# Performance work log

Measured on AMD Instinct MI355X. Metric: run time of the kernel, lower is better.

Reference implementation:

```python
import jax, jax.numpy as jnp
import numpy as np

TEMPERATURE = 0.07
EPS = 1e-12  # F.normalize clamp


def _project(x, We, be, W1, b1, W2, b2):
    # encoder Linear then projection head Linear->ReLU->Linear
    h = x @ We + be                      # [B, 512]
    h = jax.nn.relu(h @ W1 + b1)         # [B, 256]
    return h @ W2 + b2                   # [B, 128]


def _ntxent(z1, z2, t):
    B = z1.shape[0]
    z1 = z1 / jnp.maximum(jnp.linalg.norm(z1, axis=1, keepdims=True), EPS)
    z2 = z2 / jnp.maximum(jnp.linalg.norm(z2, axis=1, keepdims=True), EPS)
    reps = jnp.concatenate([z1, z2], axis=0)          # [2B, 128]
    sim = reps @ reps.T                               # [2B, 2B]
    N = 2 * B
    idx = jnp.arange(N)
    # positives: eye rolled by B along columns -> column (i+B) mod N
    pos = sim[idx, (idx + B) % N][:, None]            # [N, 1]
    # negatives: all off-diagonal entries per row, in column order
    cols = jnp.arange(N - 1)[None, :]                 # [1, N-1]
    neg_idx = cols + (cols >= idx[:, None])           # skip the diagonal
    neg = jnp.take_along_axis(sim, neg_idx, axis=1)   # [N, N-1]
    logits = jnp.concatenate([pos, neg], axis=1) / t  # [N, N]
    # cross-entropy with label 0
    return jnp.mean(jax.nn.logsumexp(logits, axis=1) - logits[:, 0])


def setup_inputs() -> dict:
    key = jax.random.key(0)
    ks = jax.random.split(key, 10)
    B, Din, Denc, Dh, Dp = 4096, 1024, 512, 256, 128
    s = lambda fan_in: 1.0 / np.sqrt(fan_in)
    return {
        "x_image": jax.random.normal(ks[0], (B, Din), jnp.float32),
        "x_text": jax.random.normal(ks[1], (B, Din), jnp.float32),
        "We_img": jax.random.normal(ks[2], (Din, Denc), jnp.float32) * s(Din),
        "be_img": jnp.zeros((Denc,), jnp.float32),
        "We_txt": jax.random.normal(ks[3], (Din, Denc), jnp.float32) * s(Din),
        "be_txt": jnp.zeros((Denc,), jnp.float32),
        "Wp1_img": jax.random.normal(ks[4], (Denc, Dh), jnp.float32) * s(Denc),
        "bp1_img": jnp.zeros((Dh,), jnp.float32),
        "Wp2_img": jax.random.normal(ks[5], (Dh, Dp), jnp.float32) * s(Dh),
        "bp2_img": jnp.zeros((Dp,), jnp.float32),
        "Wp1_txt": jax.random.normal(ks[6], (Denc, Dh), jnp.float32) * s(Denc),
        "bp1_txt": jnp.zeros((Dh,), jnp.float32),
        "Wp2_txt": jax.random.normal(ks[7], (Dh, Dp), jnp.float32) * s(Dh),
        "bp2_txt": jnp.zeros((Dp,), jnp.float32),
    }


def reference(x_image, x_text, We_img, be_img, We_txt, be_txt,
              Wp1_img, bp1_img, Wp2_img, bp2_img,
              Wp1_txt, bp1_txt, Wp2_txt, bp2_txt):
    z1 = _project(x_image, We_img, be_img, Wp1_img, bp1_img, Wp2_img, bp2_img)
    z2 = _project(x_text, We_txt, be_txt, Wp1_txt, bp1_txt, Wp2_txt, bp2_txt)
    # single modality pair ('image','text') -> one NT-Xent loss
    return _ntxent(z1, z2, TEMPERATURE)
```

## Files before the change

kernel.cpp:

```cpp
#include <hip/hip_runtime.h>
#include <hip/hip_bf16.h>
#include <math.h>

typedef __bf16 bf16_t;
typedef __bf16 bf8 __attribute__((ext_vector_type(8)));
typedef __bf16 bf4 __attribute__((ext_vector_type(4)));
typedef float f32x4 __attribute__((ext_vector_type(4)));
typedef int i32x8 __attribute__((ext_vector_type(8)));
typedef unsigned char u8;

#define AS1 __attribute__((address_space(1)))
#define AS3 __attribute__((address_space(3)))

#define B_ROWS 4096
#define NTOT   8192
#define DIN    1024
#define DENC   512
#define DH     256
#define DP     128
#define NSLICE 64
#define INV_T        14.285714285714286f
#define SCALE_LOG2   20.609929155556620f

__device__ __forceinline__ f32x4 mfma_16x16x32(bf8 a, bf8 b, f32x4 c) {
  return __builtin_amdgcn_mfma_f32_16x16x32_bf16(a, b, c, 0, 0, 0);
}

__global__ __launch_bounds__(256) void prep_kernel(
    const float* __restrict__ x_i, const float* __restrict__ x_t,
    const float* __restrict__ We_i, const float* __restrict__ We_t,
    const float* __restrict__ W1_i, const float* __restrict__ W1_t,
    const float* __restrict__ W2_i, const float* __restrict__ W2_t,
    bf16_t* __restrict__ xb_i, bf16_t* __restrict__ xb_t,
    bf16_t* __restrict__ Wet_i, bf16_t* __restrict__ Wet_t,
    bf16_t* __restrict__ W1t_i, bf16_t* __restrict__ W1t_t,
    bf16_t* __restrict__ W2t_i, bf16_t* __restrict__ W2t_t) {
  const int b = blockIdx.x;
  const int tid = threadIdx.x;
  if (b >= 336) {
    int idx = (b - 336) * 256 + tid;
    const int HALF = (B_ROWS * DIN) / 4;
    const float* s; bf16_t* d; int off;
    if (idx < HALF) { s = x_i; d = xb_i; off = idx; }
    else            { s = x_t; d = xb_t; off = idx - HALF; }
    float4 v = ((const float4*)s)[off];
    bf4 w = { (bf16_t)v.x, (bf16_t)v.y, (bf16_t)v.z, (bf16_t)v.w };
    ((bf4*)d)[off] = w;
    return;
  }
  const float* src; bf16_t* dst; int K, N, tile;
  if (b < 128)      { src = We_i; dst = Wet_i; K = 1024; N = 512; tile = b; }
  else if (b < 256) { src = We_t; dst = Wet_t; K = 1024; N = 512; tile = b - 128; }
  else if (b < 288) { src = W1_i; dst = W1t_i; K = 512;  N = 256; tile = b - 256; }
  else if (b < 320) { src = W1_t; dst = W1t_t; K = 512;  N = 256; tile = b - 288; }
  else if (b < 328) { src = W2_i; dst = W2t_i; K = 256;  N = 128; tile = b - 320; }
  else              { src = W2_t; dst = W2t_t; K = 256;  N = 128; tile = b - 328; }
  const int tilesN = N >> 6;
  const int k0 = (tile / tilesN) * 64;
  const int n0 = (tile % tilesN) * 64;

  __shared__ float ld[64][65];
  #pragma unroll
  for (int i = 0; i < 4; ++i) {
    int cid = tid + i * 256;
    int r = cid >> 4;
    int c = (cid & 15) * 4;
    float4 v = *(const float4*)(src + (size_t)(k0 + r) * N + n0 + c);
    ld[r][c + 0] = v.x; ld[r][c + 1] = v.y; ld[r][c + 2] = v.z; ld[r][c + 3] = v.w;
  }
  __syncthreads();
  #pragma unroll
  for (int i = 0; i < 2; ++i) {
    int cid = tid + i * 256;
    int rn = cid >> 3;
    int c8 = (cid & 7) * 8;
    bf8 w;
    #pragma unroll
    for (int j = 0; j < 8; ++j) w[j] = (bf16_t)ld[c8 + j][rn];
    *(bf8*)(dst + (size_t)(n0 + rn) * K + k0 + c8) = w;
  }
}

template<int MT, bool RELU>
__global__ __launch_bounds__(256) void gemm_glds(
    const bf16_t* __restrict__ A0, const bf16_t* __restrict__ A1,
    const bf16_t* __restrict__ B0, const bf16_t* __restrict__ B1,
    const float* __restrict__ bias0, const float* __restrict__ bias1,
    bf16_t* __restrict__ out0, bf16_t* __restrict__ out1,
    int N, int K) {
  const bf16_t* A   = blockIdx.z ? A1 : A0;
  const bf16_t* Bt  = blockIdx.z ? B1 : B0;
  const float* bias = blockIdx.z ? bias1 : bias0;
  bf16_t* outp      = blockIdx.z ? out1 : out0;

  const int nb   = blockIdx.x * 64;
  const int mb   = blockIdx.y * MT;
  const int tid  = threadIdx.x;
  const int wave = tid >> 6;
  const int lane = tid & 63;
  const int l15  = lane & 15;
  const int quad = lane >> 4;
  constexpr int CH = MT / 64;

  __shared__ __align__(16) bf16_t As[3][MT * 32];
  __shared__ __align__(16) bf16_t Bs[3][64 * 32];

  f32x4 acc[CH][4];
  #pragma unroll
  for (int i = 0; i < CH; ++i)
    #pragma unroll
    for (int j = 0; j < 4; ++j) acc[i][j] = (f32x4){0.f, 0.f, 0.f, 0.f};

  auto stage = [&](int k0, int pb) {
    #pragma unroll
    for (int i = 0; i < CH; ++i) {
      const int s = tid + i * 256;
      const bf16_t* ga = A + (size_t)(mb + (s >> 2)) * K + k0 + (s & 3) * 8;
      __builtin_amdgcn_global_load_lds(
          (const AS1 void*)ga,
          (AS3 void*)(As[pb] + (size_t)(wave * 64 + i * 256) * 8), 16, 0, 0);
    }
    const bf16_t* gb = Bt + (size_t)(nb + (tid >> 2)) * K + k0 + (tid & 3) * 8;
    __builtin_amdgcn_global_load_lds(
        (const AS1 void*)gb,
        (AS3 void*)(Bs[pb] + (size_t)(wave * 64) * 8), 16, 0, 0);
  };

  const int T = K >> 5;
  stage(0, 0);
  stage(32, 1);
  for (int t = 0; t < T; ++t) {
    if (t == T - 1) {
      asm volatile("s_waitcnt vmcnt(0)" ::: "memory");
    } else if constexpr (CH == 2) {
      asm volatile("s_waitcnt vmcnt(3)" ::: "memory");
    } else {
      asm volatile("s_waitcnt vmcnt(2)" ::: "memory");
    }
    __builtin_amdgcn_s_barrier();
    if (t + 2 < T) stage((t + 2) << 5, (t + 2) % 3);
    const bf16_t* as = As[t % 3];
    const bf16_t* bs = Bs[t % 3];
    bf8 a[CH];
    #pragma unroll
    for (int i = 0; i < CH; ++i)
      a[i] = *(const bf8*)(as + (size_t)(wave * (16 * CH) + i * 16 + l15) * 32 + quad * 8);
    #pragma unroll
    for (int nt = 0; nt < 4; ++nt) {
      bf8 bb = *(const bf8*)(bs + (size_t)(nt * 16 + l15) * 32 + quad * 8);
      #pragma unroll
      for (int i = 0; i < CH; ++i)
        acc[i][nt] = mfma_16x16x32(a[i], bb, acc[i][nt]);
    }
  }

  #pragma unroll
  for (int i = 0; i < CH; ++i) {
    const int orow = mb + wave * (16 * CH) + i * 16 + quad * 4;
    #pragma unroll
    for (int nt = 0; nt < 4; ++nt) {
      const int ocol = nb + nt * 16 + l15;
      const float bval = bias[ocol];
      #pragma unroll
      for (int r = 0; r < 4; ++r) {
        float v = acc[i][nt][r] + bval;
        if (RELU) v = fmaxf(v, 0.f);
        outp[(size_t)(orow + r) * N + ocol] = (bf16_t)v;
      }
    }
  }
}

__global__ __launch_bounds__(256) void head2_norm(
    const bf16_t* __restrict__ A0, const bf16_t* __restrict__ A1,
    const bf16_t* __restrict__ B0, const bf16_t* __restrict__ B1,
    const float* __restrict__ bias0, const float* __restrict__ bias1,
    u8* __restrict__ reps8) {
  const bf16_t* A   = blockIdx.z ? A1 : A0;
  const bf16_t* Bt  = blockIdx.z ? B1 : B0;
  const float* bias = blockIdx.z ? bias1 : bias0;

  const int mb   = blockIdx.x * 16;
  const int tid  = threadIdx.x;
  const int wave = tid >> 6;
  const int lane = tid & 63;
  const int l15  = lane & 15;
  const int quad = lane >> 4;
  const int wc0  = wave * 32;

  __shared__ __align__(16) bf16_t Asb[8 * 16 * 32];
  __shared__ __align__(16) bf16_t Bsb[8 * 128 * 32];
  __shared__ float ssL[64];

  #pragma unroll
  for (int i = 0; i < 2; ++i) {
    const int s = i * 256 + tid;
    const int kt = s >> 6, slot = s & 63;
    const int row = slot >> 2, j = slot & 3, cf = j ^ (row & 3);
    const bf16_t* ga = A + (size_t)(mb + row) * DH + kt * 32 + cf * 8;
    __builtin_amdgcn_global_load_lds(
        (const AS1 void*)ga,
        (AS3 void*)(Asb + (size_t)(i * 256 + wave * 64) * 8), 16, 0, 0);
  }
  #pragma unroll
  for (int i = 0; i < 16; ++i) {
    const int s2 = i * 256 + tid;
    const int kt = s2 >> 9, slot = s2 & 511;
    const int col = slot >> 2, j = slot & 3, cf = j ^ (col & 3);
    const bf16_t* gb = Bt + (size_t)col * DH + kt * 32 + cf * 8;
    __builtin_amdgcn_global_load_lds(
        (const AS1 void*)gb,
        (AS3 void*)(Bsb + (size_t)(i * 256 + wave * 64) * 8), 16, 0, 0);
  }
  __syncthreads();

  f32x4 acc[2];
  acc[0] = (f32x4){0.f, 0.f, 0.f, 0.f};
  acc[1] = (f32x4){0.f, 0.f, 0.f, 0.f};
  #pragma unroll
  for (int kt = 0; kt < 8; ++kt) {
    bf8 a = *(const bf8*)(Asb + (size_t)kt * 512 +
                          (size_t)(l15 * 4 + (quad ^ (l15 & 3))) * 8);
    #pragma unroll
    for (int nt = 0; nt < 2; ++nt) {
      const int col = wc0 + nt * 16 + l15;
      bf8 bb = *(const bf8*)(Bsb + (size_t)kt * 4096 +
                             (size_t)(col * 4 + (quad ^ (col & 3))) * 8);
      acc[nt] = mfma_16x16x32(a, bb, acc[nt]);
    }
  }

  float ssp[4];
  #pragma unroll
  for (int r = 0; r < 4; ++r) {
    #pragma unroll
    for (int nt = 0; nt < 2; ++nt) acc[nt][r] += bias[wc0 + nt * 16 + l15];
    float s = acc[0][r] * acc[0][r] + acc[1][r] * acc[1][r];
    s += __shfl_xor(s, 1); s += __shfl_xor(s, 2);
    s += __shfl_xor(s, 4); s += __shfl_xor(s, 8);
    ssp[r] = s;
  }
  if (l15 == 0) {
    #pragma unroll
    for (int r = 0; r < 4; ++r) ssL[wave * 16 + quad * 4 + r] = ssp[r];
  }
  __syncthreads();
  const size_t gr0 = (size_t)(blockIdx.z ? B_ROWS : 0) + mb + quad * 4;
  #pragma unroll
  for (int r = 0; r < 4; ++r) {
    const int row = quad * 4 + r;
    float tot = ssL[row] + ssL[16 + row] + ssL[32 + row] + ssL[48 + row];
    const float inv = 1.0f / fmaxf(sqrtf(tot), 1e-12f);
    int pk = __builtin_amdgcn_cvt_pk_fp8_f32(acc[0][r] * inv, acc[1][r] * inv, 0, 0);
    reps8[(gr0 + r) * DP + wc0 + l15]      = (u8)(pk & 0xff);
    reps8[(gr0 + r) * DP + wc0 + 16 + l15] = (u8)((pk >> 8) & 0xff);
  }
}

__global__ __launch_bounds__(256, 4) void sim_fp8_kernel(
    const u8* __restrict__ reps8, float* __restrict__ Spart) {
  const int l = blockIdx.x;
  int by = (int)((65.0f - sqrtf(4225.0f - 4.0f * (float)l)) * 0.5f);
  while ((by + 1) * (65 - (by + 1)) <= l) ++by;
  while (by * (65 - by) > l) --by;
  const int bxh = 2 * by + (l - by * (65 - by));
  const bool diag = (bxh - 2 * by) < 2;
  const int rowbase = by * 256;
  const int col0    = bxh * 128;
  const int tid  = threadIdx.x;
  const int wave = tid >> 6;
  const int lane = tid & 63;
  const int l15  = lane & 15;
  const int quad = lane >> 4;

  __shared__ __align__(16) u8 Bs[2][64 * DP];
  __shared__ float csw[4][128];

  const int r0 = rowbase + wave * 64;
  i32x8 af[4];
  #pragma unroll
  for (int c = 0; c < 4; ++c) {
    const uint4* ap = (const uint4*)(reps8 + (size_t)(r0 + c * 16 + l15) * DP + quad * 32);
    uint4 x0 = ap[0], x1 = ap[1];
    af[c] = (i32x8){(int)x0.x, (int)x0.y, (int)x0.z, (int)x0.w,
                    (int)x1.x, (int)x1.y, (int)x1.z, (int)x1.w};
  }

  float rs[4][4];
  #pragma unroll
  for (int c = 0; c < 4; ++c)
    #pragma unroll
    for (int r = 0; r < 4; ++r) rs[c][r] = 0.f;

  auto stage = [&](int t, int pb) {
    const int jt0 = col0 + t * 64;
    #pragma unroll
    for (int i = 0; i < 2; ++i) {
      const int s   = i * 256 + tid;
      const int col = s >> 3;
      const int cf  = (s & 7) ^ (col & 7);
      const u8* g = reps8 + (size_t)(jt0 + col) * DP + cf * 16;
      __builtin_amdgcn_global_load_lds(
          (const AS1 void*)g,
          (AS3 void*)(Bs[pb] + (size_t)(i * 256 + wave * 64) * 16), 16, 0, 0);
    }
  };

  stage(0, 0);
  for (int t = 0; t < 2; ++t) {
    __syncthreads();
    if (t == 0) stage(1, 1);
    const u8* buf = Bs[t & 1];

    #pragma unroll
    for (int g = 0; g < 2; ++g) {
      f32x4 pacc[2][4];
      __builtin_amdgcn_s_setprio(1);
      #pragma unroll
      for (int h = 0; h < 2; ++h) {
        const int st = g * 2 + h;
        const int coln = st * 16 + l15;
        const u8* cbase = buf + (size_t)coln * DP;
        const int c0 = ((2 * quad)     ^ (coln & 7)) * 16;
        const int c1 = ((2 * quad + 1) ^ (coln & 7)) * 16;
        uint4 b0 = *(const uint4*)(cbase + c0);
        uint4 b1 = *(const uint4*)(cbase + c1);
        i32x8 bf = (i32x8){(int)b0.x, (int)b0.y, (int)b0.z, (int)b0.w,
                           (int)b1.x, (int)b1.y, (int)b1.z, (int)b1.w};
        #pragma unroll
        for (int c = 0; c < 4; ++c) {
          pacc[h][c] = __builtin_amdgcn_mfma_scale_f32_16x16x128_f8f6f4(
              af[c], bf, (f32x4){0.f, 0.f, 0.f, 0.f}, 0, 0, 0,
              0x7F7F7F7F, 0, 0x7F7F7F7F);
        }
      }
      __builtin_amdgcn_s_setprio(0);

      #pragma unroll
      for (int h = 0; h < 2; ++h) {
        float csp[4] = {0.f, 0.f, 0.f, 0.f};
        #pragma unroll
        for (int c = 0; c < 4; ++c) {
          #pragma unroll
          for (int r = 0; r < 4; ++r) {
            float ev = __builtin_amdgcn_exp2f(pacc[h][c][r] * SCALE_LOG2);
            rs[c][r] += ev;
            csp[r] += ev;
          }
        }
        if (!diag) {
          float cs = (csp[0] + csp[1]) + (csp[2] + csp[3]);
          cs += __shfl_xor(cs, 16);
          cs += __shfl_xor(cs, 32);
          if (quad == 0) csw[wave][t * 64 + (g * 2 + h) * 16 + l15] = cs;
        }
      }
    }
  }

  #pragma unroll
  for (int c = 0; c < 4; ++c) {
    const int i0 = r0 + c * 16 + quad * 4;
    #pragma unroll
    for (int r = 0; r < 4; ++r) {
      float v = rs[c][r];
      v += __shfl_xor(v, 1); v += __shfl_xor(v, 2);
      v += __shfl_xor(v, 4); v += __shfl_xor(v, 8);
      if (l15 == 0) Spart[(size_t)bxh * NTOT + i0 + r] = v;
    }
  }

  if (!diag) {
    __syncthreads();
    if (tid < 128) {
      Spart[(size_t)(2 * by) * NTOT + col0 + tid] = csw[0][tid] + csw[1][tid];
    } else {
      const int j = tid - 128;
      Spart[(size_t)(2 * by + 1) * NTOT + col0 + j] = csw[2][j] + csw[3][j];
    }
  }
}

__global__ __launch_bounds__(256) void rowfinal_kernel(
    const u8* __restrict__ reps8, const float* __restrict__ Spart,
    float* __restrict__ L) {
  const int tid  = threadIdx.x;
  const int wave = tid >> 6;
  const int lane = tid & 63;
  const int row  = blockIdx.x * 4 + wave;
  const int ua = *(const unsigned short*)(reps8 + (size_t)row * DP + lane * 2);
  const int ub = *(const unsigned short*)(reps8 + (size_t)(row ^ B_ROWS) * DP + lane * 2);
  float a0 = __builtin_amdgcn_cvt_f32_fp8(ua, 0);
  float a1 = __builtin_amdgcn_cvt_f32_fp8(ua, 1);
  float b0 = __builtin_amdgcn_cvt_f32_fp8(ub, 0);
  float b1 = __builtin_amdgcn_cvt_f32_fp8(ub, 1);
  float dii = a0 * a0 + a1 * a1;
  float pos = a0 * b0 + a1 * b1;
  float ps  = Spart[(size_t)lane * NTOT + row];
  #pragma unroll
  for (int m = 1; m < 64; m <<= 1) {
    dii += __shfl_xor(dii, m);
    pos += __shfl_xor(pos, m);
    ps  += __shfl_xor(ps, m);
  }
  if (lane == 0) {
    float Si = ps - __builtin_amdgcn_exp2f(dii * SCALE_LOG2)
                  + __builtin_amdgcn_exp2f(pos * SCALE_LOG2);
    L[row] = logf(Si) - pos * INV_T;
  }
}

__global__ __launch_bounds__(1024) void reduce_kernel(
    const float* __restrict__ L, float* __restrict__ out) {
  const int tid = threadIdx.x;
  float acc = 0.f;
  for (int i = tid; i < NTOT; i += 1024) acc += L[i];
  #pragma unroll
  for (int m = 1; m < 64; m <<= 1) acc += __shfl_xor(acc, m);
  __shared__ float wsum[16];
  if ((tid & 63) == 0) wsum[tid >> 6] = acc;
  __syncthreads();
  if (tid < 16) {
    float v = wsum[tid];
    #pragma unroll
    for (int m = 1; m < 16; m <<= 1) v += __shfl_xor(v, m);
    if (tid == 0) out[0] = v * (1.0f / NTOT);
  }
}

extern "C" void kernel_launch(void* const* d_in, const int* in_sizes, int n_in,
                              void* d_out, int out_size, void* d_ws, size_t ws_size,
                              hipStream_t stream) {
  const float* x_img  = (const float*)d_in[0];
  const float* x_txt  = (const float*)d_in[1];
  const float* We_img = (const float*)d_in[2];
  const float* be_img = (const float*)d_in[3];
  const float* We_txt = (const float*)d_in[4];
  const float* be_txt = (const float*)d_in[5];
  const float* W1_img = (const float*)d_in[6];
  const float* b1_img = (const float*)d_in[7];
  const float* W2_img = (const float*)d_in[8];
  const float* b2_img = (const float*)d_in[9];
  const float* W1_txt = (const float*)d_in[10];
  const float* b1_txt = (const float*)d_in[11];
  const float* W2_txt = (const float*)d_in[12];
  const float* b2_txt = (const float*)d_in[13];

  char* p = (char*)d_ws;
  bf16_t* xbf_img = (bf16_t*)p; p += (size_t)B_ROWS * DIN * 2;
  bf16_t* xbf_txt = (bf16_t*)p; p += (size_t)B_ROWS * DIN * 2;
  bf16_t* Wet_img = (bf16_t*)p; p += (size_t)DENC * DIN * 2;
  bf16_t* Wet_txt = (bf16_t*)p; p += (size_t)DENC * DIN * 2;
  bf16_t* W1t_img = (bf16_t*)p; p += (size_t)DH * DENC * 2;
  bf16_t* W1t_txt = (bf16_t*)p; p += (size_t)DH * DENC * 2;
  bf16_t* W2t_img = (bf16_t*)p; p += (size_t)DP * DH * 2;
  bf16_t* W2t_txt = (bf16_t*)p; p += (size_t)DP * DH * 2;
  bf16_t* h_img   = (bf16_t*)p; p += (size_t)B_ROWS * DENC * 2;
  bf16_t* h_txt   = (bf16_t*)p; p += (size_t)B_ROWS * DENC * 2;
  bf16_t* g_img   = (bf16_t*)p; p += (size_t)B_ROWS * DH * 2;
  bf16_t* g_txt   = (bf16_t*)p; p += (size_t)B_ROWS * DH * 2;
  u8*     reps8   = (u8*)    p; p += (size_t)NTOT * DP;
  float*  Spart   = (float*) p; p += (size_t)NSLICE * NTOT * 4;
  float*  L       = (float*) p; p += (size_t)NTOT * 4;

  prep_kernel<<<336 + 8192, 256, 0, stream>>>(
      x_img, x_txt, We_img, We_txt, W1_img, W1_txt, W2_img, W2_txt,
      xbf_img, xbf_txt, Wet_img, Wet_txt, W1t_img, W1t_txt, W2t_img, W2t_txt);

  gemm_glds<128, false><<<dim3(DENC / 64, B_ROWS / 128, 2), 256, 0, stream>>>(
      xbf_img, xbf_txt, Wet_img, Wet_txt, be_img, be_txt, h_img, h_txt,
      DENC, DIN);
  gemm_glds<64, true><<<dim3(DH / 64, B_ROWS / 64, 2), 256, 0, stream>>>(
      h_img, h_txt, W1t_img, W1t_txt, b1_img, b1_txt, g_img, g_txt,
      DH, DENC);
  head2_norm<<<dim3(B_ROWS / 16, 1, 2), 256, 0, stream>>>(
      g_img, g_txt, W2t_img, W2t_txt, b2_img, b2_txt, reps8);

  sim_fp8_kernel<<<dim3(1056), 256, 0, stream>>>(reps8, Spart);
  rowfinal_kernel<<<NTOT / 4, 256, 0, stream>>>(reps8, Spart, L);
  reduce_kernel<<<1, 1024, 0, stream>>>(L, (float*)d_out);
}
```

Measured before the change: 182.2 us.

## Fuse projection head layers, fold final reduction into rowfinal, coarsen cast blocks

Merges the W1 GEMM+ReLU and the W2 GEMM+normalize into one per-16-row kernel that keeps the hidden activation in LDS, so the intermediate g tensor is never written to or read from global memory. The final mean reduction moves into the rowfinal kernel through a last-block atomic counter, which removes a launch but adds a memset. The input cast now processes four float4 elements per thread with a quarter of the blocks. The fused head kernel uses small 16-row tiles and reloads the full W1 for every block, and it synchronizes on each k-step, which may leave the MFMA units underused.

```diff
diff --git a/kernel.cpp b/kernel.cpp
--- a/kernel.cpp
+++ b/kernel.cpp
@@ -25,6 +25,7 @@
 __device__ __forceinline__ f32x4 mfma_16x16x32(bf8 a, bf8 b, f32x4 c) {
   return __builtin_amdgcn_mfma_f32_16x16x32_bf16(a, b, c, 0, 0, 0);
 }
+
 
 __global__ __launch_bounds__(256) void prep_kernel(
     const float* __restrict__ x_i, const float* __restrict__ x_t,
@@ -38,14 +39,18 @@
   const int b = blockIdx.x;
   const int tid = threadIdx.x;
   if (b >= 336) {
-    int idx = (b - 336) * 256 + tid;
+    const int base = (b - 336) * 256 + tid;
     const int HALF = (B_ROWS * DIN) / 4;
-    const float* s; bf16_t* d; int off;
-    if (idx < HALF) { s = x_i; d = xb_i; off = idx; }
-    else            { s = x_t; d = xb_t; off = idx - HALF; }
-    float4 v = ((const float4*)s)[off];
-    bf4 w = { (bf16_t)v.x, (bf16_t)v.y, (bf16_t)v.z, (bf16_t)v.w };
-    ((bf4*)d)[off] = w;
+    #pragma unroll
+    for (int it = 0; it < 4; ++it) {
+      int idx = base + it * (2048 * 256);
+      const float* s; bf16_t* d; int off;
+      if (idx < HALF) { s = x_i; d = xb_i; off = idx; }
+      else            { s = x_t; d = xb_t; off = idx - HALF; }
+      float4 v = ((const float4*)s)[off];
+      bf4 w = { (bf16_t)v.x, (bf16_t)v.y, (bf16_t)v.z, (bf16_t)v.w };
+      ((bf4*)d)[off] = w;
+    }
     return;
   }
   const float* src; bf16_t* dst; int K, N, tile;
@@ -132,10 +137,9 @@
   for (int t = 0; t < T; ++t) {
     if (t == T - 1) {
       asm volatile("s_waitcnt vmcnt(0)" ::: "memory");
-    } else if constexpr (CH == 2) {
-      asm volatile("s_waitcnt vmcnt(3)" ::: "memory");
     } else {
-      asm volatile("s_waitcnt vmcnt(2)" ::: "memory");
+      if constexpr (CH == 2) asm volatile("s_waitcnt vmcnt(3)" ::: "memory");
+      else                   asm volatile("s_waitcnt vmcnt(2)" ::: "memory");
     }
     __builtin_amdgcn_s_barrier();
     if (t + 2 < T) stage((t + 2) << 5, (t + 2) % 3);
@@ -171,62 +175,112 @@
   }
 }
 
-__global__ __launch_bounds__(256) void head2_norm(
-    const bf16_t* __restrict__ A0, const bf16_t* __restrict__ A1,
-    const bf16_t* __restrict__ B0, const bf16_t* __restrict__ B1,
-    const float* __restrict__ bias0, const float* __restrict__ bias1,
+__global__ __launch_bounds__(256) void head12_norm(
+    const bf16_t* __restrict__ h_i, const bf16_t* __restrict__ h_t,
+    const bf16_t* __restrict__ W1t_i, const bf16_t* __restrict__ W1t_t,
+    const bf16_t* __restrict__ W2t_i, const bf16_t* __restrict__ W2t_t,
+    const float* __restrict__ b1_i, const float* __restrict__ b1_t,
+    const float* __restrict__ b2_i, const float* __restrict__ b2_t,
     u8* __restrict__ reps8) {
-  const bf16_t* A   = blockIdx.z ? A1 : A0;
-  const bf16_t* Bt  = blockIdx.z ? B1 : B0;
-  const float* bias = blockIdx.z ? bias1 : bias0;
-
-  const int mb   = blockIdx.x * 16;
+  const int z  = blockIdx.z;
+  const int mb = blockIdx.x * 16;
+  const bf16_t* H   = z ? h_t : h_i;
+  const bf16_t* W1t = z ? W1t_t : W1t_i;
+  const bf16_t* W2t = z ? W2t_t : W2t_i;
+  const float*  b1  = z ? b1_t : b1_i;
+  const float*  b2  = z ? b2_t : b2_i;
+
   const int tid  = threadIdx.x;
   const int wave = tid >> 6;
   const int lane = tid & 63;
   const int l15  = lane & 15;
   const int quad = lane >> 4;
-  const int wc0  = wave * 32;
-
-  __shared__ __align__(16) bf16_t Asb[8 * 16 * 32];
-  __shared__ __align__(16) bf16_t Bsb[8 * 128 * 32];
+
+  __shared__ __align__(16) bf16_t As[16 * 512];
+  __shared__ __align__(16) bf16_t B1s[2][256 * 32];
+  __shared__ __align__(16) bf16_t G[16 * 264];
+  __shared__ __align__(16) bf16_t B2s[2][128 * 32];
   __shared__ float ssL[64];
 
   #pragma unroll
-  for (int i = 0; i < 2; ++i) {
+  for (int i = 0; i < 4; ++i) {
     const int s = i * 256 + tid;
-    const int kt = s >> 6, slot = s & 63;
-    const int row = slot >> 2, j = slot & 3, cf = j ^ (row & 3);
-    const bf16_t* ga = A + (size_t)(mb + row) * DH + kt * 32 + cf * 8;
+    const int kt = s >> 6, rem = s & 63, row = rem >> 2, j = rem & 3;
+    const int cf = j ^ (row & 3);
+    const bf16_t* ga = H + (size_t)(mb + row) * DENC + kt * 32 + cf * 8;
     __builtin_amdgcn_global_load_lds(
-        (const AS1 void*)ga,
-        (AS3 void*)(Asb + (size_t)(i * 256 + wave * 64) * 8), 16, 0, 0);
-  }
-  #pragma unroll
-  for (int i = 0; i < 16; ++i) {
-    const int s2 = i * 256 + tid;
-    const int kt = s2 >> 9, slot = s2 & 511;
-    const int col = slot >> 2, j = slot & 3, cf = j ^ (col & 3);
-    const bf16_t* gb = Bt + (size_t)col * DH + kt * 32 + cf * 8;
-    __builtin_amdgcn_global_load_lds(
-        (const AS1 void*)gb,
-        (AS3 void*)(Bsb + (size_t)(i * 256 + wave * 64) * 8), 16, 0, 0);
-  }
-  __syncthreads();
-
-  f32x4 acc[2];
-  acc[0] = (f32x4){0.f, 0.f, 0.f, 0.f};
-  acc[1] = (f32x4){0.f, 0.f, 0.f, 0.f};
-  #pragma unroll
-  for (int kt = 0; kt < 8; ++kt) {
-    bf8 a = *(const bf8*)(Asb + (size_t)kt * 512 +
+        (const AS1 void*)ga, (AS3 void*)(As + (size_t)(i * 256 + wave * 64) * 8),
+        16, 0, 0);
+  }
+  auto stage_w1 = [&](int kt, int pb) {
+    #pragma unroll
+    for (int i = 0; i < 4; ++i) {
+      const int s = i * 256 + tid;
+      const int col = s >> 2, j = s & 3, cf = j ^ (col & 3);
+      const bf16_t* gb = W1t + (size_t)col * DENC + kt * 32 + cf * 8;
+      __builtin_amdgcn_global_load_lds(
+          (const AS1 void*)gb,
+          (AS3 void*)(B1s[pb] + (size_t)(i * 256 + wave * 64) * 8), 16, 0, 0);
+    }
+  };
+
+  stage_w1(0, 0);
+  f32x4 acc1[4];
+  #pragma unroll
+  for (int nt = 0; nt < 4; ++nt) acc1[nt] = (f32x4){0.f, 0.f, 0.f, 0.f};
+  const int wc0 = wave * 64;
+  for (int kt = 0; kt < 16; ++kt) {
+    __syncthreads();
+    if (kt < 15) stage_w1(kt + 1, (kt + 1) & 1);
+    const bf16_t* bs = B1s[kt & 1];
+    bf8 a = *(const bf8*)(As + (size_t)kt * 512 +
                           (size_t)(l15 * 4 + (quad ^ (l15 & 3))) * 8);
     #pragma unroll
+    for (int nt = 0; nt < 4; ++nt) {
+      const int col = wc0 + nt * 16 + l15;
+      bf8 bb = *(const bf8*)(bs + (size_t)(col * 4 + (quad ^ (col & 3))) * 8);
+      acc1[nt] = mfma_16x16x32(a, bb, acc1[nt]);
+    }
+  }
+
+  auto stage_w2 = [&](int kt2, int pb) {
+    #pragma unroll
+    for (int i = 0; i < 2; ++i) {
+      const int s = i * 256 + tid;
+      const int col = s >> 2, j = s & 3, cf = j ^ (col & 3);
+      const bf16_t* gb = W2t + (size_t)col * DH + kt2 * 32 + cf * 8;
+      __builtin_amdgcn_global_load_lds(
+          (const AS1 void*)gb,
+          (AS3 void*)(B2s[pb] + (size_t)(i * 256 + wave * 64) * 8), 16, 0, 0);
+    }
+  };
+  stage_w2(0, 0);
+
+  #pragma unroll
+  for (int nt = 0; nt < 4; ++nt) {
+    const int col = wc0 + nt * 16 + l15;
+    const float bv = b1[col];
+    #pragma unroll
+    for (int r = 0; r < 4; ++r) {
+      float v = fmaxf(acc1[nt][r] + bv, 0.f);
+      G[(size_t)(quad * 4 + r) * 264 + col] = (bf16_t)v;
+    }
+  }
+
+  f32x4 acc2[2];
+  acc2[0] = (f32x4){0.f, 0.f, 0.f, 0.f};
+  acc2[1] = (f32x4){0.f, 0.f, 0.f, 0.f};
+  const int wc2 = wave * 32;
+  for (int kt2 = 0; kt2 < 8; ++kt2) {
+    __syncthreads();
+    if (kt2 < 7) stage_w2(kt2 + 1, (kt2 + 1) & 1);
+    const bf16_t* bs = B2s[kt2 & 1];
+    bf8 a = *(const bf8*)(G + (size_t)l15 * 264 + kt2 * 32 + quad * 8);
+    #pragma unroll
     for (int nt = 0; nt < 2; ++nt) {
-      const int col = wc0 + nt * 16 + l15;
-      bf8 bb = *(const bf8*)(Bsb + (size_t)kt * 4096 +
-                             (size_t)(col * 4 + (quad ^ (col & 3))) * 8);
-      acc[nt] = mfma_16x16x32(a, bb, acc[nt]);
+      const int col = wc2 + nt * 16 + l15;
+      bf8 bb = *(const bf8*)(bs + (size_t)(col * 4 + (quad ^ (col & 3))) * 8);
+      acc2[nt] = mfma_16x16x32(a, bb, acc2[nt]);
     }
   }
 
@@ -234,8 +288,8 @@
   #pragma unroll
   for (int r = 0; r < 4; ++r) {
     #pragma unroll
-    for (int nt = 0; nt < 2; ++nt) acc[nt][r] += bias[wc0 + nt * 16 + l15];
-    float s = acc[0][r] * acc[0][r] + acc[1][r] * acc[1][r];
+    for (int nt = 0; nt < 2; ++nt) acc2[nt][r] += b2[wc2 + nt * 16 + l15];
+    float s = acc2[0][r] * acc2[0][r] + acc2[1][r] * acc2[1][r];
     s += __shfl_xor(s, 1); s += __shfl_xor(s, 2);
     s += __shfl_xor(s, 4); s += __shfl_xor(s, 8);
     ssp[r] = s;
@@ -245,15 +299,15 @@
     for (int r = 0; r < 4; ++r) ssL[wave * 16 + quad * 4 + r] = ssp[r];
   }
   __syncthreads();
-  const size_t gr0 = (size_t)(blockIdx.z ? B_ROWS : 0) + mb + quad * 4;
+  const size_t gr0 = (size_t)(z ? B_ROWS : 0) + mb + quad * 4;
   #pragma unroll
   for (int r = 0; r < 4; ++r) {
     const int row = quad * 4 + r;
     float tot = ssL[row] + ssL[16 + row] + ssL[32 + row] + ssL[48 + row];
     const float inv = 1.0f / fmaxf(sqrtf(tot), 1e-12f);
-    int pk = __builtin_amdgcn_cvt_pk_fp8_f32(acc[0][r] * inv, acc[1][r] * inv, 0, 0);
-    reps8[(gr0 + r) * DP + wc0 + l15]      = (u8)(pk & 0xff);
-    reps8[(gr0 + r) * DP + wc0 + 16 + l15] = (u8)((pk >> 8) & 0xff);
+    int pk = __builtin_amdgcn_cvt_pk_fp8_f32(acc2[0][r] * inv, acc2[1][r] * inv, 0, 0);
+    reps8[(gr0 + r) * DP + wc2 + l15]      = (u8)(pk & 0xff);
+    reps8[(gr0 + r) * DP + wc2 + 16 + l15] = (u8)((pk >> 8) & 0xff);
   }
 }
 
@@ -381,9 +435,10 @@
   }
 }
 
-__global__ __launch_bounds__(256) void rowfinal_kernel(
+__global__ __launch_bounds__(256) void rowfinal_reduce(
     const u8* __restrict__ reps8, const float* __restrict__ Spart,
-    float* __restrict__ L) {
+    float* __restrict__ partials, unsigned* __restrict__ syncc,
+    float* __restrict__ out) {
   const int tid  = threadIdx.x;
   const int wave = tid >> 6;
   const int lane = tid & 63;
@@ -403,28 +458,34 @@
     pos += __shfl_xor(pos, m);
     ps  += __shfl_xor(ps, m);
   }
+  __shared__ float ws[4];
+  __shared__ int isLast;
   if (lane == 0) {
     float Si = ps - __builtin_amdgcn_exp2f(dii * SCALE_LOG2)
                   + __builtin_amdgcn_exp2f(pos * SCALE_LOG2);
-    L[row] = logf(Si) - pos * INV_T;
-  }
-}
-
-__global__ __launch_bounds__(1024) void reduce_kernel(
-    const float* __restrict__ L, float* __restrict__ out) {
-  const int tid = threadIdx.x;
-  float acc = 0.f;
-  for (int i = tid; i < NTOT; i += 1024) acc += L[i];
-  #pragma unroll
-  for (int m = 1; m < 64; m <<= 1) acc += __shfl_xor(acc, m);
-  __shared__ float wsum[16];
-  if ((tid & 63) == 0) wsum[tid >> 6] = acc;
+    ws[wave] = logf(Si) - pos * INV_T;
+  }
   __syncthreads();
-  if (tid < 16) {
-    float v = wsum[tid];
-    #pragma unroll
-    for (int m = 1; m < 16; m <<= 1) v += __shfl_xor(v, m);
-    if (tid == 0) out[0] = v * (1.0f / NTOT);
+  if (tid == 0) {
+    float p = (ws[0] + ws[1]) + (ws[2] + ws[3]);
+    __hip_atomic_store(&partials[blockIdx.x], p, __ATOMIC_RELAXED,
+                       __HIP_MEMORY_SCOPE_AGENT);
+    unsigned prev = __hip_atomic_fetch_add(&syncc[0], 1u, __ATOMIC_ACQ_REL,
+                                           __HIP_MEMORY_SCOPE_AGENT);
+    isLast = (prev == (unsigned)(NTOT / 4 - 1));
+  }
+  __syncthreads();
+  if (isLast) {
+    float s = 0.f;
+    for (int i = tid; i < NTOT / 4; i += 256)
+      s += __hip_atomic_load(&partials[i], __ATOMIC_RELAXED,
+                             __HIP_MEMORY_SCOPE_AGENT);
+    #pragma unroll
+    for (int m = 1; m < 64; m <<= 1) s += __shfl_xor(s, m);
+    __shared__ float w2[4];
+    if (lane == 0) w2[wave] = s;
+    __syncthreads();
+    if (tid == 0) out[0] = ((w2[0] + w2[1]) + (w2[2] + w2[3])) * (1.0f / NTOT);
   }
 }
 
@@ -457,26 +518,25 @@
   bf16_t* W2t_txt = (bf16_t*)p; p += (size_t)DP * DH * 2;
   bf16_t* h_img   = (bf16_t*)p; p += (size_t)B_ROWS * DENC * 2;
   bf16_t* h_txt   = (bf16_t*)p; p += (size_t)B_ROWS * DENC * 2;
-  bf16_t* g_img   = (bf16_t*)p; p += (size_t)B_ROWS * DH * 2;
-  bf16_t* g_txt   = (bf16_t*)p; p += (size_t)B_ROWS * DH * 2;
   u8*     reps8   = (u8*)    p; p += (size_t)NTOT * DP;
   float*  Spart   = (float*) p; p += (size_t)NSLICE * NTOT * 4;
-  float*  L       = (float*) p; p += (size_t)NTOT * 4;
-
-  prep_kernel<<<336 + 8192, 256, 0, stream>>>(
+  float*  partials= (float*) p; p += (size_t)(NTOT / 4) * 4;
+  unsigned* syncc = (unsigned*)p; p += 64;
+
+  hipMemsetAsync((void*)syncc, 0, 64, stream);
+
+  prep_kernel<<<336 + 2048, 256, 0, stream>>>(
       x_img, x_txt, We_img, We_txt, W1_img, W1_txt, W2_img, W2_txt,
       xbf_img, xbf_txt, Wet_img, Wet_txt, W1t_img, W1t_txt, W2t_img, W2t_txt);
 
   gemm_glds<128, false><<<dim3(DENC / 64, B_ROWS / 128, 2), 256, 0, stream>>>(
       xbf_img, xbf_txt, Wet_img, Wet_txt, be_img, be_txt, h_img, h_txt,
       DENC, DIN);
-  gemm_glds<64, true><<<dim3(DH / 64, B_ROWS / 64, 2), 256, 0, stream>>>(
-      h_img, h_txt, W1t_img, W1t_txt, b1_img, b1_txt, g_img, g_txt,
-      DH, DENC);
-  head2_norm<<<dim3(B_ROWS / 16, 1, 2), 256, 0, stream>>>(
-      g_img, g_txt, W2t_img, W2t_txt, b2_img, b2_txt, reps8);
+  head12_norm<<<dim3(B_ROWS / 16, 1, 2), 256, 0, stream>>>(
+      h_img, h_txt, W1t_img, W1t_txt, W2t_img, W2t_txt,
+      b1_img, b1_txt, b2_img, b2_txt, reps8);
 
   sim_fp8_kernel<<<dim3(1056), 256, 0, stream>>>(reps8, Spart);
-  rowfinal_kernel<<<NTOT / 4, 256, 0, stream>>>(reps8, Spart, L);
-  reduce_kernel<<<1, 1024, 0, stream>>>(L, (float*)d_out);
-}
+  rowfinal_reduce<<<NTOT / 4, 256, 0, stream>>>(
+      reps8, Spart, partials, syncc, (float*)d_out);
+}
```

Result: slower. 235.6 us (+29.3%).
